# Kernel tuning notes

Measured on AMD Instinct MI355X. Metric: run time of the kernel, lower is better.

Reference implementation:

```python
import jax, jax.numpy as jnp
import numpy as np

EMBED = 128
HEADS = 16
N = 10000
E = 160000
NEG_SLOPE = 0.2


def setup_inputs() -> dict:
    key = jax.random.key(0)
    ks = jax.random.split(key, 12)
    s = 0.05
    return {
        "x": jax.random.normal(ks[0], (N, EMBED), jnp.float32),
        "edge_index": jax.random.randint(ks[1], (2, E), 0, N, jnp.int64),
        # gat1: in=EMBED, out=EMBED, heads=16, concat
        "W1": jax.random.normal(ks[2], (EMBED, HEADS * EMBED), jnp.float32) * s,
        "a_src1": jax.random.normal(ks[3], (HEADS, EMBED), jnp.float32) * s,
        "a_dst1": jax.random.normal(ks[4], (HEADS, EMBED), jnp.float32) * s,
        "b1": jnp.zeros((HEADS * EMBED,), jnp.float32),
        # gat2: in=HEADS*EMBED, out=EMBED, heads=1, no concat
        "W2": jax.random.normal(ks[5], (HEADS * EMBED, EMBED), jnp.float32) * s,
        "a_src2": jax.random.normal(ks[6], (1, EMBED), jnp.float32) * s,
        "a_dst2": jax.random.normal(ks[7], (1, EMBED), jnp.float32) * s,
        "b2": jnp.zeros((EMBED,), jnp.float32),
        # classifier
        "Wc": jax.random.normal(ks[8], (EMBED, 1), jnp.float32) * s,
        "bc": jnp.zeros((1,), jnp.float32),
    }


def _gat_layer(x, src, dst, W, a_src, a_dst, b, heads, out_ch, n_nodes):
    # node projection: [N, H, C]
    h = (x @ W).reshape(n_nodes, heads, out_ch)
    # per-node attention logits [N, H]
    al_s = jnp.einsum('nhc,hc->nh', h, a_src)
    al_d = jnp.einsum('nhc,hc->nh', h, a_dst)
    # per-edge logits [E, H]
    e = jax.nn.leaky_relu(al_s[src] + al_d[dst], NEG_SLOPE)
    # segment softmax over incoming edges of each dst node
    m = jax.ops.segment_max(e, dst, num_segments=n_nodes)
    ex = jnp.exp(e - m[dst])
    z = jax.ops.segment_sum(ex, dst, num_segments=n_nodes)
    alpha = ex / (z[dst] + 1e-16)
    # weighted scatter-aggregate [N, H, C]
    msg = h[src] * alpha[:, :, None]
    out = jax.ops.segment_sum(msg, dst, num_segments=n_nodes)
    return out.reshape(n_nodes, heads * out_ch) + b


def reference(x, edge_index, W1, a_src1, a_dst1, b1, W2, a_src2, a_dst2, b2, Wc, bc):
    n_nodes = x.shape[0]
    # PyG GATConv default: add self loops
    loop = jnp.arange(n_nodes, dtype=edge_index.dtype)
    src = jnp.concatenate([edge_index[0], loop])
    dst = jnp.concatenate([edge_index[1], loop])
    h = _gat_layer(x, src, dst, W1, a_src1, a_dst1, b1, HEADS, EMBED, n_nodes)
    h = jax.nn.elu(h)
    h = _gat_layer(h, src, dst, W2, a_src2, a_dst2, b2, 1, EMBED, n_nodes)
    return h @ Wc + bc  # [N, 1]
```

## Files before the change

### kernel.cpp

```cpp
#include <hip/hip_runtime.h>
#include <hip/hip_bf16.h>

#define EMBED 128
#define HEADS 16
#define NEG 0.2f

typedef __attribute__((ext_vector_type(8))) short short8;
typedef __attribute__((ext_vector_type(4))) float floatx4;

static __device__ __forceinline__ float leaky(float x) { return x > 0.f ? x : NEG * x; }

static __device__ __forceinline__ short f2bf_bits(float f) {
  __hip_bfloat16 h = __float2bfloat16(f);
  union { __hip_bfloat16 b; short s; } u;
  u.b = h;
  return u.s;
}


__global__ void k_hist(const int* __restrict__ ei, int E, int N, int* __restrict__ deg) {
  int i = blockIdx.x * blockDim.x + threadIdx.x;
  int Et = E + N;
  if (i >= Et) return;
  int d = (i < E) ? ei[E + i] : (i - E);
  atomicAdd(&deg[d], 1);
}

__global__ __launch_bounds__(256) void k_scan1(const int* __restrict__ deg,
                                               int* __restrict__ excl,
                                               int* __restrict__ bsum, int n) {
  __shared__ int s[256];
  int i = blockIdx.x * 256 + threadIdx.x;
  int v = (i < n) ? deg[i] : 0;
  s[threadIdx.x] = v;
  __syncthreads();
  for (int d = 1; d < 256; d <<= 1) {
    int add = ((int)threadIdx.x >= d) ? s[threadIdx.x - d] : 0;
    __syncthreads();
    s[threadIdx.x] += add;
    __syncthreads();
  }
  if (i < n) excl[i] = s[threadIdx.x] - v;
  if (threadIdx.x == 255) bsum[blockIdx.x] = s[255];
}

__global__ void k_scan2(int* __restrict__ bsum, int nb) {
  if (threadIdx.x == 0 && blockIdx.x == 0) {
    int acc = 0;
    for (int i = 0; i < nb; ++i) { int v = bsum[i]; bsum[i] = acc; acc += v; }
  }
}

__global__ __launch_bounds__(256) void k_scan3(const int* __restrict__ deg,
                                               const int* __restrict__ excl,
                                               const int* __restrict__ bsum,
                                               int* __restrict__ row_ptr,
                                               int* __restrict__ cursor, int n) {
  int i = blockIdx.x * 256 + threadIdx.x;
  if (i < n) {
    int r = excl[i] + bsum[blockIdx.x];
    row_ptr[i] = r;
    cursor[i] = r;
    if (i == n - 1) row_ptr[n] = r + deg[i];
  }
}

__global__ void k_scatter(const int* __restrict__ ei, int E, int N,
                          int* __restrict__ cursor, int* __restrict__ csr_src) {
  int i = blockIdx.x * blockDim.x + threadIdx.x;
  int Et = E + N;
  if (i >= Et) return;
  int s = (i < E) ? ei[i] : (i - E);
  int d = (i < E) ? ei[E + i] : (i - E);
  int pos = atomicAdd(&cursor[d], 1);
  csr_src[pos] = s;
}


__global__ __launch_bounds__(256) void k_prepAll(const float* __restrict__ W1,
                                                 const float* __restrict__ a_src1,
                                                 const float* __restrict__ a_dst1,
                                                 const float* __restrict__ W2,
                                                 const float* __restrict__ a_src2,
                                                 const float* __restrict__ a_dst2,
                                                 const float* __restrict__ Wc,
                                                 const float* __restrict__ b2,
                                                 const float* __restrict__ bc,
                                                 float* __restrict__ wsAll,
                                                 float* __restrict__ uvec,
                                                 float* __restrict__ cconst) {
  int gid = blockIdx.x * 256 + threadIdx.x;
  if (gid < 4096) {
    int sel = gid >> 11;
    int id = gid & 2047;
    int h = id >> 7, k = id & 127;
    const float* av = sel ? a_dst1 : a_src1;
    float sum = 0.f;
    const float* wrow = W1 + (size_t)k * 2048 + h * 128;
    const float* arow = av + h * 128;
#pragma unroll 4
    for (int c = 0; c < 128; ++c) sum += wrow[c] * arow[c];
    wsAll[gid] = sum;
  } else if (gid < 10240) {
    int g = gid - 4096;
    int sel = g >> 11;
    int k = g & 2047;
    const float* v = sel == 0 ? Wc : (sel == 1 ? a_src2 : a_dst2);
    const float* wrow = W2 + (size_t)k * 128;
    float s = 0.f;
#pragma unroll 4
    for (int j = 0; j < 128; ++j) s += wrow[j] * v[j];
    uvec[g] = s;
  } else if (gid == 10240) {
    float s = 0.f;
    for (int j = 0; j < 128; ++j) s += b2[j] * Wc[j];
    *cconst = s + bc[0];
  }
}


__global__ __launch_bounds__(256) void k_prep2aT(const float* __restrict__ W1,
                                                 short* __restrict__ hi,
                                                 short* __restrict__ lo) {
  __shared__ float tile[64][65];
  int h = blockIdx.x;
  int c0 = blockIdx.y * 64;
  int j0 = blockIdx.z * 64;
  int t = threadIdx.x;
#pragma unroll
  for (int i = 0; i < 4; ++i) {
    int idx4 = i * 256 + t;
    int c = idx4 >> 4, j4 = idx4 & 15;
    float4 v = *(const float4*)&W1[(size_t)(c0 + c) * 2048 + h * 128 + j0 + j4 * 4];
    tile[c][j4 * 4 + 0] = v.x;
    tile[c][j4 * 4 + 1] = v.y;
    tile[c][j4 * 4 + 2] = v.z;
    tile[c][j4 * 4 + 3] = v.w;
  }
  __syncthreads();
#pragma unroll
  for (int i = 0; i < 4; ++i) {
    int idx = i * 256 + t;
    int j = idx >> 4, c4 = idx & 15;
    unsigned short vh[4], vl[4];
#pragma unroll
    for (int ii = 0; ii < 4; ++ii) {
      float wv = tile[c4 * 4 + ii][j];
      short hb = f2bf_bits(wv);
      float hf = __uint_as_float(((unsigned int)(unsigned short)hb) << 16);
      vh[ii] = (unsigned short)hb;
      vl[ii] = (unsigned short)f2bf_bits(wv - hf);
    }
    size_t o = (size_t)h * 16384 + (size_t)(j0 + j) * 128 + c0 + c4 * 4;
    *(ushort4*)&hi[o] = make_ushort4(vh[0], vh[1], vh[2], vh[3]);
    *(ushort4*)&lo[o] = make_ushort4(vl[0], vl[1], vl[2], vl[3]);
  }
}


__global__ __launch_bounds__(256) void k_al1v2(const float* __restrict__ x,
                                               const float* __restrict__ wsAll,
                                               float* __restrict__ als,
                                               float* __restrict__ ald, int N) {
  __shared__ float wss[128][16], wsd[128][16];
  int tid = threadIdx.x;
  for (int i = tid; i < 2048; i += 256) {
    int h = i >> 7, c = i & 127;
    wss[c][h] = wsAll[i];
    wsd[c][h] = wsAll[2048 + i];
  }
  __syncthreads();
  int gid = blockIdx.x * 256 + tid;
  int n = gid >> 4, h = gid & 15;
  if (n >= N) return;
  const float4* xp = (const float4*)(x + (size_t)n * 128);
  float ps = 0.f, pd = 0.f;
#pragma unroll 8
  for (int c4 = 0; c4 < 32; ++c4) {
    float4 xv = xp[c4];
    int c = c4 * 4;
    ps += xv.x * wss[c][h] + xv.y * wss[c + 1][h] + xv.z * wss[c + 2][h] + xv.w * wss[c + 3][h];
    pd += xv.x * wsd[c][h] + xv.y * wsd[c + 1][h] + xv.z * wsd[c + 2][h] + xv.w * wsd[c + 3][h];
  }
  als[gid] = ps;
  ald[gid] = pd;
}


__global__ __launch_bounds__(256) void k_attn1w(const float* __restrict__ x,
                                                const float* __restrict__ als,
                                                const float* __restrict__ ald,
                                                const int* __restrict__ row_ptr,
                                                const int* __restrict__ csr,
                                                __hip_bfloat16* __restrict__ xaggb,
                                                int N) {
  int tid = threadIdx.x;
  int d = blockIdx.x * 4 + (tid >> 6);
  if (d >= N) return;
  int lane = tid & 63;
  int h = lane & 15, es = lane >> 4;
  int grp = lane & 48;

  int e0 = row_ptr[d];
  int deg = row_ptr[d + 1] - e0;

  float aldh = ald[(size_t)d * 16 + h];

  float zp = 0.f;
  for (int e = es; e < deg; e += 4) {
    int s = csr[e0 + e];
    zp += __expf(leaky(als[(size_t)s * 16 + h] + aldh));
  }
  zp += __shfl_xor(zp, 16);
  zp += __shfl_xor(zp, 32);
  float iz = 1.f / (zp + 1e-16f);

  float accx[16], accy[16];
#pragma unroll
  for (int k = 0; k < 16; ++k) { accx[k] = 0.f; accy[k] = 0.f; }

  const float* xc = x + lane * 2;
  for (int e = 0; e < deg; ++e) {
    int s = csr[e0 + e];
    float ev = __expf(leaky(als[(size_t)s * 16 + h] + aldh)) * iz;
    float2 xv = *(const float2*)(xc + (size_t)s * 128);
#pragma unroll
    for (int k = 0; k < 16; ++k) {
      float a = __shfl(ev, grp | k);
      accx[k] += a * xv.x;
      accy[k] += a * xv.y;
    }
  }

  __hip_bfloat16* op = xaggb + (size_t)d * 128 + lane * 2;
#pragma unroll
  for (int k = 0; k < 16; ++k) {
    __hip_bfloat16 t[2];
    t[0] = __float2bfloat16(accx[k]);
    t[1] = __float2bfloat16(accy[k]);
    *(unsigned int*)(op + (size_t)k * N * 128) = *(unsigned int*)t;
  }
}


__global__ __launch_bounds__(256, 2) void k_fused(const __hip_bfloat16* __restrict__ xaggb,
                                                  const short* __restrict__ w1t_hi,
                                                  const short* __restrict__ w1t_lo,
                                                  const float* __restrict__ b1,
                                                  const float* __restrict__ uvec,
                                                  float* __restrict__ partc,
                                                  float* __restrict__ parts,
                                                  float* __restrict__ partd,
                                                  int N) {
  __shared__ float sh[512];
  __shared__ __align__(16) char Bh[32768];
  __shared__ __align__(16) char Bl[32768];
  int tid = threadIdx.x;
  int h = blockIdx.y;
  int n0 = blockIdx.x * 256;

  for (int i = tid; i < 512; i += 256) {
    int arr = i >> 7, jj = i & 127;
    sh[i] = (arr == 0) ? b1[h * 128 + jj] : uvec[(arr - 1) * 2048 + h * 128 + jj];
  }
  const char* gbh = (const char*)(w1t_hi + (size_t)h * 16384);
  const char* gbl = (const char*)(w1t_lo + (size_t)h * 16384);
#pragma unroll
  for (int i = 0; i < 8; ++i) {
    int ci = i * 256 + tid;
    int row = ci >> 4, kc = ci & 15;
    int po = row * 256 + ((kc ^ (row & 15)) << 4);
    *(uint4*)(Bh + po) = *(const uint4*)(gbh + ci * 16);
    *(uint4*)(Bl + po) = *(const uint4*)(gbl + ci * 16);
  }

  int w = tid >> 6, lane = tid & 63;
  int quad = lane >> 4, l15 = lane & 15;
  int nw = n0 + w * 64;

  const char* abase = (const char*)xaggb + (size_t)h * N * 256;
  short8 a[4][4];
#pragma unroll
  for (int nt = 0; nt < 4; ++nt) {
    int node = nw + nt * 16 + l15;
    if (node >= N) node = N - 1;
    const char* rowp = abase + (size_t)node * 256 + quad * 16;
#pragma unroll
    for (int ks = 0; ks < 4; ++ks)
      a[nt][ks] = *(const short8*)(rowp + ks * 64);
  }
  __syncthreads();

  floatx4 acc[4][8];
#pragma unroll
  for (int jt = 0; jt < 8; ++jt) {
    floatx4 bb = *(const floatx4*)&sh[jt * 16 + quad * 4];
#pragma unroll
    for (int nt = 0; nt < 4; ++nt) acc[nt][jt] = bb;
  }

  for (int ks = 0; ks < 4; ++ks) {
    int xo = (((ks * 4 + quad) ^ l15) << 4);
#pragma unroll
    for (int jt = 0; jt < 8; ++jt) {
      int po = (jt * 16 + l15) * 256 + xo;
      short8 wh = *(const short8*)(Bh + po);
      short8 wl = *(const short8*)(Bl + po);
#pragma unroll
      for (int nt = 0; nt < 4; ++nt) {
        acc[nt][jt] = __builtin_amdgcn_mfma_f32_16x16x32_bf16(wh, a[nt][ks], acc[nt][jt], 0, 0, 0);
        acc[nt][jt] = __builtin_amdgcn_mfma_f32_16x16x32_bf16(wl, a[nt][ks], acc[nt][jt], 0, 0, 0);
      }
    }
  }

  float pc[4] = {0.f, 0.f, 0.f, 0.f};
  float ps[4] = {0.f, 0.f, 0.f, 0.f};
  float pd[4] = {0.f, 0.f, 0.f, 0.f};
#pragma unroll
  for (int jt = 0; jt < 8; ++jt) {
    floatx4 uc = *(const floatx4*)&sh[128 + jt * 16 + quad * 4];
    floatx4 us = *(const floatx4*)&sh[256 + jt * 16 + quad * 4];
    floatx4 ud = *(const floatx4*)&sh[384 + jt * 16 + quad * 4];
#pragma unroll
    for (int nt = 0; nt < 4; ++nt) {
#pragma unroll
      for (int r = 0; r < 4; ++r) {
        float v = acc[nt][jt][r];
        float e = v > 0.f ? v : (__expf(v) - 1.f);
        pc[nt] += e * uc[r];
        ps[nt] += e * us[r];
        pd[nt] += e * ud[r];
      }
    }
  }
#pragma unroll
  for (int nt = 0; nt < 4; ++nt) {
    float c = pc[nt], s = ps[nt], dd = pd[nt];
    c += __shfl_xor(c, 16); c += __shfl_xor(c, 32);
    s += __shfl_xor(s, 16); s += __shfl_xor(s, 32);
    dd += __shfl_xor(dd, 16); dd += __shfl_xor(dd, 32);
    int node = nw + nt * 16 + l15;
    if (quad == 0 && node < N) {
      atomicAdd(&partc[node], c);
      atomicAdd(&parts[node], s);
      atomicAdd(&partd[node], dd);
    }
  }
}


__global__ __launch_bounds__(256) void k_attn2s(const float* __restrict__ partc,
                                                const float* __restrict__ parts,
                                                const float* __restrict__ partd,
                                                const int* __restrict__ row_ptr,
                                                const int* __restrict__ csr,
                                                const float* __restrict__ cconst,
                                                float* __restrict__ out, int N) {
  int w = threadIdx.x >> 6, lane = threadIdx.x & 63;
  int d = blockIdx.x * 4 + w;
  if (d >= N) return;
  int e0 = row_ptr[d], deg = row_ptr[d + 1] - e0;
  float aldd = partd[d];
  float z = 0.f, num = 0.f;
  for (int e = lane; e < deg; e += 64) {
    int s = csr[e0 + e];
    float v = __expf(leaky(parts[s] + aldd));
    z += v;
    num += v * partc[s];
  }
#pragma unroll
  for (int off = 32; off; off >>= 1) {
    z += __shfl_xor(z, off);
    num += __shfl_xor(num, off);
  }
  if (lane == 0) out[d] = num / (z + 1e-16f) + cconst[0];
}


extern "C" void kernel_launch(void* const* d_in, const int* in_sizes, int n_in,
                              void* d_out, int out_size, void* d_ws, size_t ws_size,
                              hipStream_t stream) {
  const float* x      = (const float*)d_in[0];
  const int*   ei     = (const int*)d_in[1];
  const float* W1     = (const float*)d_in[2];
  const float* a_src1 = (const float*)d_in[3];
  const float* a_dst1 = (const float*)d_in[4];
  const float* b1     = (const float*)d_in[5];
  const float* W2     = (const float*)d_in[6];
  const float* a_src2 = (const float*)d_in[7];
  const float* a_dst2 = (const float*)d_in[8];
  const float* b2     = (const float*)d_in[9];
  const float* Wc     = (const float*)d_in[10];
  const float* bc     = (const float*)d_in[11];

  int N = in_sizes[0] / EMBED;
  int E = in_sizes[1] / 2;
  int Et = E + N;
  int nScanB = (N + 255) / 256;

  char* ws = (char*)d_ws;
  size_t off = 0;
  auto alloc = [&](size_t bytes) -> void* {
    void* p = ws + off;
    off += (bytes + 255) & ~(size_t)255;
    return p;
  };
  __hip_bfloat16* xaggb = (__hip_bfloat16*)alloc((size_t)N * 2048 * 2 + 65536);
  short* w1t_hi = (short*)alloc((size_t)262144 * 2);
  short* w1t_lo = (short*)alloc((size_t)262144 * 2);
  float* wsAll  = (float*)alloc(4096 * 4);
  float* uvec   = (float*)alloc(6144 * 4);
  float* cconst = (float*)alloc(256);
  float* als1   = (float*)alloc((size_t)N * 16 * 4);
  float* ald1   = (float*)alloc((size_t)N * 16 * 4);
  float* part   = (float*)alloc((size_t)3 * N * 4);
  float* partc  = part;
  float* parts  = part + N;
  float* partd  = part + 2 * N;
  int* deg      = (int*)alloc((size_t)N * 4);
  int* excl     = (int*)alloc((size_t)N * 4);
  int* bsum     = (int*)alloc((size_t)(nScanB + 1) * 4);
  int* row_ptr  = (int*)alloc((size_t)(N + 1) * 4);
  int* cursor   = (int*)alloc((size_t)N * 4);
  int* csr      = (int*)alloc((size_t)Et * 4);

  hipMemsetAsync(deg, 0, (size_t)N * 4, stream);
  hipMemsetAsync(part, 0, (size_t)3 * N * 4, stream);

  k_hist<<<(Et + 255) / 256, 256, 0, stream>>>(ei, E, N, deg);
  k_scan1<<<nScanB, 256, 0, stream>>>(deg, excl, bsum, N);
  k_scan2<<<1, 64, 0, stream>>>(bsum, nScanB);
  k_scan3<<<nScanB, 256, 0, stream>>>(deg, excl, bsum, row_ptr, cursor, N);
  k_scatter<<<(Et + 255) / 256, 256, 0, stream>>>(ei, E, N, cursor, csr);

  k_prepAll<<<41, 256, 0, stream>>>(W1, a_src1, a_dst1, W2, a_src2, a_dst2, Wc, b2, bc,
                                    wsAll, uvec, cconst);
  k_prep2aT<<<dim3(16, 2, 2), 256, 0, stream>>>(W1, w1t_hi, w1t_lo);

  k_al1v2<<<(N * 16 + 255) / 256, 256, 0, stream>>>(x, wsAll, als1, ald1, N);
  k_attn1w<<<(N + 3) / 4, 256, 0, stream>>>(x, als1, ald1, row_ptr, csr, xaggb, N);

  k_fused<<<dim3((N + 255) / 256, 16), 256, 0, stream>>>(xaggb, w1t_hi, w1t_lo, b1, uvec,
                                                         partc, parts, partd, N);
  k_attn2s<<<(N + 3) / 4, 256, 0, stream>>>(partc, parts, partd, row_ptr, csr, cconst,
                                            (float*)d_out, N);
}
```

Measured before the change: 203.7 us.

## Remap attention-aggregation lanes to head×quarter-row and drop per-edge shuffles

The layer-1 attention aggregation kernel used to give each lane two feature columns and broadcast all 16 head weights through 16 shuffles per edge. Now each lane owns one head and a 32-column quarter of the source row. It computes its own edge weight, loads the row slice with float4 reads, processes two edges per iteration, and writes 16-byte bf16 stores after one final normalisation. This removes the shuffle traffic and the per-edge normalisation multiply. In exchange the same x row is loaded redundantly by all 16 head groups, the loads are less coalesced per wavefront, and register pressure is higher.

```diff
diff --git a/kernel.cpp b/kernel.cpp
--- a/kernel.cpp
+++ b/kernel.cpp
@@ -187,7 +187,7 @@
 }
 
 
-__global__ __launch_bounds__(256) void k_attn1w(const float* __restrict__ x,
+__global__ __launch_bounds__(256) void k_attn1e(const float* __restrict__ x,
                                                 const float* __restrict__ als,
                                                 const float* __restrict__ ald,
                                                 const int* __restrict__ row_ptr,
@@ -198,47 +198,69 @@
   int d = blockIdx.x * 4 + (tid >> 6);
   if (d >= N) return;
   int lane = tid & 63;
-  int h = lane & 15, es = lane >> 4;
-  int grp = lane & 48;
+  int h = lane >> 2, sub = lane & 3;
 
   int e0 = row_ptr[d];
   int deg = row_ptr[d + 1] - e0;
-
   float aldh = ald[(size_t)d * 16 + h];
 
   float zp = 0.f;
-  for (int e = es; e < deg; e += 4) {
+  for (int e = sub; e < deg; e += 4) {
     int s = csr[e0 + e];
     zp += __expf(leaky(als[(size_t)s * 16 + h] + aldh));
   }
-  zp += __shfl_xor(zp, 16);
-  zp += __shfl_xor(zp, 32);
+  zp += __shfl_xor(zp, 1);
+  zp += __shfl_xor(zp, 2);
   float iz = 1.f / (zp + 1e-16f);
 
-  float accx[16], accy[16];
-#pragma unroll
-  for (int k = 0; k < 16; ++k) { accx[k] = 0.f; accy[k] = 0.f; }
-
-  const float* xc = x + lane * 2;
-  for (int e = 0; e < deg; ++e) {
-    int s = csr[e0 + e];
-    float ev = __expf(leaky(als[(size_t)s * 16 + h] + aldh)) * iz;
-    float2 xv = *(const float2*)(xc + (size_t)s * 128);
-#pragma unroll
-    for (int k = 0; k < 16; ++k) {
-      float a = __shfl(ev, grp | k);
-      accx[k] += a * xv.x;
-      accy[k] += a * xv.y;
-    }
-  }
-
-  __hip_bfloat16* op = xaggb + (size_t)d * 128 + lane * 2;
-#pragma unroll
-  for (int k = 0; k < 16; ++k) {
-    __hip_bfloat16 t[2];
-    t[0] = __float2bfloat16(accx[k]);
-    t[1] = __float2bfloat16(accy[k]);
-    *(unsigned int*)(op + (size_t)k * N * 128) = *(unsigned int*)t;
+  float4 acc[8];
+#pragma unroll
+  for (int i = 0; i < 8; ++i) acc[i] = make_float4(0.f, 0.f, 0.f, 0.f);
+
+  const float* xc = x + sub * 32;
+  int e = 0;
+  for (; e + 2 <= deg; e += 2) {
+    int s0 = csr[e0 + e];
+    int s1 = csr[e0 + e + 1];
+    float ev0 = __expf(leaky(als[(size_t)s0 * 16 + h] + aldh));
+    float ev1 = __expf(leaky(als[(size_t)s1 * 16 + h] + aldh));
+    const float4* xp0 = (const float4*)(xc + (size_t)s0 * 128);
+    const float4* xp1 = (const float4*)(xc + (size_t)s1 * 128);
+    float4 v0[8], v1[8];
+#pragma unroll
+    for (int i = 0; i < 8; ++i) v0[i] = xp0[i];
+#pragma unroll
+    for (int i = 0; i < 8; ++i) v1[i] = xp1[i];
+#pragma unroll
+    for (int i = 0; i < 8; ++i) {
+      acc[i].x += ev0 * v0[i].x; acc[i].y += ev0 * v0[i].y;
+      acc[i].z += ev0 * v0[i].z; acc[i].w += ev0 * v0[i].w;
+      acc[i].x += ev1 * v1[i].x; acc[i].y += ev1 * v1[i].y;
+      acc[i].z += ev1 * v1[i].z; acc[i].w += ev1 * v1[i].w;
+    }
+  }
+  if (e < deg) {
+    int s0 = csr[e0 + e];
+    float ev0 = __expf(leaky(als[(size_t)s0 * 16 + h] + aldh));
+    const float4* xp0 = (const float4*)(xc + (size_t)s0 * 128);
+#pragma unroll
+    for (int i = 0; i < 8; ++i) {
+      float4 v = xp0[i];
+      acc[i].x += ev0 * v.x; acc[i].y += ev0 * v.y;
+      acc[i].z += ev0 * v.z; acc[i].w += ev0 * v.w;
+    }
+  }
+
+  __hip_bfloat16* op = xaggb + (size_t)h * N * 128 + (size_t)d * 128 + sub * 32;
+#pragma unroll
+  for (int i = 0; i < 4; ++i) {
+    __hip_bfloat16 t[8];
+    float4 a0 = acc[i * 2], a1 = acc[i * 2 + 1];
+    t[0] = __float2bfloat16(a0.x * iz); t[1] = __float2bfloat16(a0.y * iz);
+    t[2] = __float2bfloat16(a0.z * iz); t[3] = __float2bfloat16(a0.w * iz);
+    t[4] = __float2bfloat16(a1.x * iz); t[5] = __float2bfloat16(a1.y * iz);
+    t[6] = __float2bfloat16(a1.z * iz); t[7] = __float2bfloat16(a1.w * iz);
+    *(uint4*)(op + i * 8) = *(uint4*)t;
   }
 }
 
@@ -439,7 +461,7 @@
   k_prep2aT<<<dim3(16, 2, 2), 256, 0, stream>>>(W1, w1t_hi, w1t_lo);
 
   k_al1v2<<<(N * 16 + 255) / 256, 256, 0, stream>>>(x, wsAll, als1, ald1, N);
-  k_attn1w<<<(N + 3) / 4, 256, 0, stream>>>(x, als1, ald1, row_ptr, csr, xaggb, N);
+  k_attn1e<<<(N + 3) / 4, 256, 0, stream>>>(x, als1, ald1, row_ptr, csr, xaggb, N);
 
   k_fused<<<dim3((N + 255) / 256, 16), 256, 0, stream>>>(xaggb, w1t_hi, w1t_lo, b1, uvec,
                                                          partc, parts, partd, N);
```

New measurement: 333.6 us. +63.7%, slower.
